# Kernel tuning notes

Hardware: AMD Instinct MI355X
Metric: run time of the kernel (lower is better)

The kernel has to match this reference:

```python
import jax, jax.numpy as jnp
import numpy as np

PERSON_DIM = 64
NUM_ZONES = 64
T_STEPS = 65536
N_EDGES = 512
H1, H2 = 128, 64
PENALTY = 1.0  # training_step=0 -> progress=0 -> penalty = min_penalty = 1.0


def build_adjacency(edge_index, num_zones):
    # symmetric 0/1 adjacency with self loops, as in set_graph_data
    A = jnp.zeros((num_zones, num_zones), jnp.float32)
    A = A.at[edge_index[0], edge_index[1]].set(1.0)
    A = A.at[edge_index[1], edge_index[0]].set(1.0)
    return jnp.maximum(A, jnp.eye(num_zones, dtype=jnp.float32))


def setup_inputs() -> dict:
    key = jax.random.key(0)
    ks = jax.random.split(key, 10)
    person_attrs = jax.random.normal(ks[0], (PERSON_DIM,), jnp.float32)
    times = jax.random.uniform(ks[1], (T_STEPS,), jnp.float32)
    zone_features = jax.random.normal(ks[2], (NUM_ZONES, 16), jnp.float32)
    edge_index = jax.random.randint(ks[3], (2, N_EDGES), 0, NUM_ZONES, jnp.int64 if jax.config.jax_enable_x64 else jnp.int32)
    din = PERSON_DIM + 1
    W1 = jax.random.normal(ks[4], (din, H1), jnp.float32) / np.sqrt(din)
    b1 = jnp.zeros((H1,), jnp.float32)
    W2 = jax.random.normal(ks[5], (H1, H2), jnp.float32) / np.sqrt(H1)
    b2 = jnp.zeros((H2,), jnp.float32)
    W3 = jax.random.normal(ks[6], (H2, NUM_ZONES), jnp.float32) / np.sqrt(H2)
    b3 = jnp.zeros((NUM_ZONES,), jnp.float32)
    return {"person_attrs": person_attrs, "times": times, "zone_features": zone_features,
            "edge_index": edge_index, "W1": W1, "b1": b1, "W2": W2, "b2": b2, "W3": W3, "b3": b3}


def reference(person_attrs, times, zone_features, edge_index, W1, b1, W2, b2, W3, b3):
    # MLP input per step = [person_attrs, time]; independent of the recurrence,
    # so batch the 3-layer MLP over all T timesteps (dropout in eval mode = identity).
    T = times.shape[0]
    x = jnp.concatenate([jnp.broadcast_to(person_attrs, (T, person_attrs.shape[0])),
                         times[:, None]], axis=-1)          # [T, D+1]
    h = jax.nn.relu(x @ W1 + b1)                              # [T, 128]
    h = jax.nn.relu(h @ W2 + b2)                              # [T, 64]
    raw_logits = h @ W3 + b3                                  # [T, Z]

    A = build_adjacency(edge_index, raw_logits.shape[-1])

    def step(current_zone, logits):
        constrained = logits - PENALTY * (1.0 - A[current_zone])
        return jnp.argmax(constrained), constrained

    _, zone_logits = jax.lax.scan(step, jnp.asarray(0, jnp.int32), raw_logits)
    return zone_logits  # [T, Z] (original also returns a None placeholder)
```

## Files before the change

kernel.cpp:

```cpp
#include <hip/hip_runtime.h>

#define T_STEPS 65536
#define NZ 64
#define NH1 128
#define NH2 64
#define NEDGE 512
#define NCHUNK 8192
#define CL 8
#define NSUPER 128
#define SUP_L 64

#define ADJ_OFF        0
#define BASE1_OFF      512
#define W1T_OFF        1536
#define NBRP_OFF       2560
#define DEGS_OFF       6656
#define CHUNKSTATE_OFF 6720
#define B2D_OFF        139264
#define B3D_OFF        139776
#define LG32_OFF       140288
#define FTAB_OFF       (LG32_OFF + (size_t)T_STEPS * NZ * 4)

#define CHUNKG_DOUT    0
#define SUPERS_DOUT    524288

typedef unsigned long long ull;
typedef unsigned int u32;
typedef unsigned char u8;
typedef double f64x4 __attribute__((ext_vector_type(4)));

__global__ void prep_kernel(const float* __restrict__ pa,
                            const int* __restrict__ edges,
                            const float* __restrict__ W1,
                            const float* __restrict__ b1,
                            const float* __restrict__ b2,
                            const float* __restrict__ b3,
                            unsigned char* ws) {
  ull* adj = (ull*)(ws + ADJ_OFF);
  double* base1 = (double*)(ws + BASE1_OFF);
  double* w1t   = (double*)(ws + W1T_OFF);
  double* b2d = (double*)(ws + B2D_OFF);
  double* b3d = (double*)(ws + B3D_OFF);
  int tid = threadIdx.x;
  if (tid < NZ) adj[tid] = 0ull;
  __syncthreads();
  if (tid < NEDGE) {
    int e0 = edges[tid];
    int e1 = edges[NEDGE + tid];
    atomicOr(&adj[e0], 1ull << e1);
    atomicOr(&adj[e1], 1ull << e0);
  }
  if (tid < NZ) atomicOr(&adj[tid], 1ull << tid);
  if (tid < NH1) {
    double acc = (double)b1[tid];
    for (int d = 0; d < 64; ++d)
      acc += (double)pa[d] * (double)W1[d * NH1 + tid];
    base1[tid] = acc;
    w1t[tid] = (double)W1[64 * NH1 + tid];
  }
  if (tid < NH2) b2d[tid] = (double)b2[tid];
  if (tid < NZ)  b3d[tid] = (double)b3[tid];
  __syncthreads();
  if (tid < NZ) {
    ull m = adj[tid];
    u32 wbuf[16];
    #pragma unroll
    for (int i = 0; i < 16; ++i) wbuf[i] = 0u;
    int deg = 0, jfirst = 0;
    while (m) {
      int j = __builtin_ctzll(m);
      m &= m - 1;
      if (deg == 0) jfirst = j;
      wbuf[deg >> 2] |= (u32)j << ((deg & 3) * 8);
      ++deg;
    }
    int padded = (deg + 3) & ~3;
    for (int k = deg; k < padded; ++k)
      wbuf[k >> 2] |= (u32)jfirst << ((k & 3) * 8);
    u32* np = (u32*)(ws + NBRP_OFF) + tid * 16;
    #pragma unroll
    for (int i = 0; i < 16; ++i) np[i] = wbuf[i];
    (ws + DEGS_OFF)[tid] = (u8)(padded >> 2);
  }
}

__global__ __launch_bounds__(512) void mlp_tables_kernel(
    const float* __restrict__ times,
    const float* __restrict__ W2,
    const float* __restrict__ W3,
    const unsigned char* __restrict__ ws_ro,
    float* __restrict__ lg32,
    unsigned char* __restrict__ chunkG,
    unsigned char* __restrict__ ftab) {
  __shared__ double region1[4224];
  __shared__ double region2[2112];
  __shared__ double base1s[NH1], w1ts[NH1];

  float* w2s = (float*)region1;
  float* w3s = (float*)region2;
  double* h2t = region1;
  double* lgT = region1;
  u8* F_lds = (u8*)region2;
  double* pv = (double*)((u8*)region2 + 4352);
  u8* pi = (u8*)region2 + 8448;

  const double* __restrict__ b2dg = (const double*)(ws_ro + B2D_OFF);
  const double* __restrict__ b3dg = (const double*)(ws_ro + B3D_OFF);

  int tid = threadIdx.x, lane = tid & 63, wv = tid >> 6;
  int i15 = lane & 15, g = lane >> 4;
  int mt = wv & 3, nt0 = (wv >> 2) * 2;
  int t0 = blockIdx.x * 64;

  for (int i = tid; i < NH1 * 64; i += 512) w2s[(i >> 6) * 66 + (i & 63)] = W2[i];
  for (int i = tid; i < NH2 * 64; i += 512) w3s[(i >> 6) * 66 + (i & 63)] = W3[i];
  if (tid < NH1) {
    base1s[tid] = ((const double*)(ws_ro + BASE1_OFF))[tid];
    w1ts[tid]   = ((const double*)(ws_ro + W1T_OFF))[tid];
  }
  double tv = (double)times[t0 + mt * 16 + i15];
  double bi20 = b2dg[nt0 * 16 + i15], bi21 = b2dg[nt0 * 16 + 16 + i15];
  double bi30 = b3dg[nt0 * 16 + i15], bi31 = b3dg[nt0 * 16 + 16 + i15];
  __syncthreads();

  f64x4 c0, c1;
  c0[0] = bi20; c0[1] = bi20; c0[2] = bi20; c0[3] = bi20;
  c1[0] = bi21; c1[1] = bi21; c1[2] = bi21; c1[3] = bi21;
  #pragma unroll 8
  for (int ks = 0; ks < 32; ++ks) {
    int h = ks * 4 + g;
    double a = fma(tv, w1ts[h], base1s[h]);
    a = a > 0.0 ? a : 0.0;
    double b0 = (double)w2s[h * 66 + nt0 * 16 + i15];
    double b1 = (double)w2s[h * 66 + nt0 * 16 + 16 + i15];
    c0 = __builtin_amdgcn_mfma_f64_16x16x4f64(a, b0, c0, 0, 0, 0);
    c1 = __builtin_amdgcn_mfma_f64_16x16x4f64(a, b1, c1, 0, 0, 0);
  }
  __syncthreads();
  #pragma unroll
  for (int r = 0; r < 4; ++r) {
    int t = mt * 16 + g * 4 + r;
    double v0 = c0[r] > 0.0 ? c0[r] : 0.0;
    double v1 = c1[r] > 0.0 ? c1[r] : 0.0;
    h2t[t * 66 + nt0 * 16 + i15] = v0;
    h2t[t * 66 + nt0 * 16 + 16 + i15] = v1;
  }
  __syncthreads();

  f64x4 d0, d1;
  d0[0] = bi30; d0[1] = bi30; d0[2] = bi30; d0[3] = bi30;
  d1[0] = bi31; d1[1] = bi31; d1[2] = bi31; d1[3] = bi31;
  #pragma unroll 8
  for (int ks = 0; ks < 16; ++ks) {
    int k = ks * 4 + g;
    double a3 = h2t[(mt * 16 + i15) * 66 + k];
    double b0 = (double)w3s[k * 66 + nt0 * 16 + i15];
    double b1 = (double)w3s[k * 66 + nt0 * 16 + 16 + i15];
    d0 = __builtin_amdgcn_mfma_f64_16x16x4f64(a3, b0, d0, 0, 0, 0);
    d1 = __builtin_amdgcn_mfma_f64_16x16x4f64(a3, b1, d1, 0, 0, 0);
  }
  __syncthreads();
  #pragma unroll
  for (int r = 0; r < 4; ++r) {
    int t = mt * 16 + g * 4 + r;
    int z0 = nt0 * 16 + i15, z1 = z0 + 16;
    lgT[z0 * 66 + t] = d0[r];
    lgT[z1 * 66 + t] = d1[r];
  }
  __syncthreads();

  {
    int zb = wv * 8;
    double vm = lgT[zb * 66 + lane];
    int jm = zb;
    lg32[(size_t)zb * T_STEPS + t0 + lane] = (float)vm;
    #pragma unroll
    for (int zz = 1; zz < 8; ++zz) {
      double v = lgT[(zb + zz) * 66 + lane];
      lg32[(size_t)(zb + zz) * T_STEPS + t0 + lane] = (float)v;
      if (v > vm) { vm = v; jm = zb + zz; }
    }
    pv[wv * 64 + lane] = vm;
    pi[wv * 64 + lane] = (u8)jm;
  }
  __syncthreads();
  double vmax = pv[lane];
  int jmax = pi[lane];
  #pragma unroll
  for (int w = 1; w < 8; ++w) {
    double v = pv[w * 64 + lane];
    int j = pi[w * 64 + lane];
    if (v > vmax) { vmax = v; jmax = j; }
  }
  double vgap = vmax - 1.0;

  const u32* __restrict__ nbrP = (const u32*)(ws_ro + NBRP_OFF);
  const u8* __restrict__ degs = ws_ro + DEGS_OFF;
  const ull* __restrict__ adjg = (const ull*)(ws_ro + ADJ_OFF);
  #pragma unroll
  for (int zz = 0; zz < 8; ++zz) {
    int z = __builtin_amdgcn_readfirstlane(wv * 8 + zz);
    ull az = adjg[z];
    int nk4 = __builtin_amdgcn_readfirstlane((int)degs[z]);
    double vn = -1.0e300;
    int jn = 0;
    for (int k4 = 0; k4 < nk4; ++k4) {
      u32 w4 = nbrP[z * 16 + k4];
      #pragma unroll
      for (int b = 0; b < 4; ++b) {
        int j = (w4 >> (b * 8)) & 63;
        double val = lgT[j * 66 + lane];
        if (val > vn) { vn = val; jn = j; }
      }
    }
    int bit = (int)((az >> jmax) & 1ull);
    int fnb = (vn > vgap) ? jn : ((vn < vgap) ? jmax : (jn < jmax ? jn : jmax));
    F_lds[lane * 68 + z] = (u8)(bit ? jmax : fnb);
  }
  __syncthreads();

  u32* fo = (u32*)(ftab + (size_t)t0 * 64);
  #pragma unroll
  for (int r = 0; r < 2; ++r) {
    int i = tid + r * 512;
    int t = i >> 4, z4 = (i & 15) << 2;
    fo[i] = *(const u32*)&F_lds[t * 68 + z4];
  }

  int c = blockIdx.x * 8 + wv;
  int cur = lane;
  #pragma unroll
  for (int i = 0; i < CL; ++i) cur = F_lds[(wv * 8 + i) * 68 + cur];
  chunkG[(size_t)c * 64 + lane] = (u8)cur;
}

__global__ __launch_bounds__(256) void super_compose_kernel(
    const unsigned char* __restrict__ chunkG,
    unsigned char* __restrict__ superS) {
  __shared__ u8 g[4][SUP_L * 64];
  int tid = threadIdx.x, lane = tid & 63, wv = tid >> 6;
  int k = blockIdx.x * 4 + wv;
  const u32* src = (const u32*)(chunkG + (size_t)k * SUP_L * 64);
  u32* dst = (u32*)g[wv];
  #pragma unroll 4
  for (int i = lane; i < SUP_L * 16; i += 64) dst[i] = src[i];
  int cur = lane;
  #pragma unroll 8
  for (int c = 0; c < SUP_L; ++c) {
    int gg = g[wv][c * 64 + lane];
    cur = __shfl(gg, cur, 64);
  }
  superS[(size_t)k * 64 + lane] = (u8)cur;
}

__global__ __launch_bounds__(256) void chunk_states_kernel(
    const unsigned char* __restrict__ chunkG,
    const unsigned char* __restrict__ superS,
    int* __restrict__ chunkState) {
  __shared__ unsigned char ssup[NSUPER * 64];
  __shared__ unsigned char g[4][SUP_L * 64];
  __shared__ int sbuf[4][SUP_L];
  int tid = threadIdx.x, lane = tid & 63, wv = tid >> 6;
  int k = blockIdx.x * 4 + wv;
  for (int i = tid; i < NSUPER * 16; i += 256)
    ((u32*)ssup)[i] = ((const u32*)superS)[i];
  const unsigned int* src = (const unsigned int*)(chunkG + (size_t)k * SUP_L * 64);
  unsigned int* dst = (unsigned int*)g[wv];
  #pragma unroll 4
  for (int i = lane; i < SUP_L * 16; i += 64) dst[i] = src[i];
  __syncthreads();
  int s = 0;
  for (int i = 0; i < k; ++i) s = ssup[i * 64 + s];
  for (int c = 0; c < SUP_L; ++c) {
    if (lane == 0) sbuf[wv][c] = s;
    s = g[wv][c * 64 + s];
  }
  chunkState[k * SUP_L + lane] = sbuf[wv][lane];
}

__global__ __launch_bounds__(256) void finalize_kernel(
    const float* __restrict__ lg32, const unsigned char* __restrict__ ws_ro,
    const int* __restrict__ chunkState, const unsigned char* __restrict__ ftab,
    float* __restrict__ out) {
  __shared__ ull adjs[64];
  __shared__ unsigned char fstage[4][CL * 64];
  int tid = threadIdx.x, lane = tid & 63, wv = tid >> 6;
  if (tid < 64) adjs[tid] = ((const ull*)(ws_ro + ADJ_OFF))[tid];
  __syncthreads();
  int c = blockIdx.x * 4 + wv;
  int s = chunkState[c];
  size_t tb = (size_t)c * CL * 64;

  float lgv[CL];
  #pragma unroll
  for (int i = 0; i < CL; ++i)
    lgv[i] = lg32[(size_t)lane * T_STEPS + c * CL + i];

  unsigned int* dst = (unsigned int*)fstage[wv];
  const unsigned int* src = (const unsigned int*)(ftab + tb);
  #pragma unroll
  for (int i = lane; i < CL * 16; i += 64) dst[i] = src[i];
  #pragma unroll
  for (int i = 0; i < CL; ++i) {
    int bit = (int)((adjs[s] >> lane) & 1ull);
    out[tb + i * 64 + lane] = bit ? lgv[i] : lgv[i] - 1.0f;
    s = fstage[wv][i * 64 + s];
  }
}

extern "C" void kernel_launch(void* const* d_in, const int* in_sizes, int n_in,
                              void* d_out, int out_size, void* d_ws, size_t ws_size,
                              hipStream_t stream) {
  const float* pa    = (const float*)d_in[0];
  const float* times = (const float*)d_in[1];
  const int*   edges = (const int*)d_in[3];
  const float* W1    = (const float*)d_in[4];
  const float* b1    = (const float*)d_in[5];
  const float* W2    = (const float*)d_in[6];
  const float* b2    = (const float*)d_in[7];
  const float* W3    = (const float*)d_in[8];
  const float* b3    = (const float*)d_in[9];

  unsigned char* ws = (unsigned char*)d_ws;
  unsigned char* outb = (unsigned char*)d_out;
  float* lg32 = (float*)(ws + LG32_OFF);
  unsigned char* ftab = ws + FTAB_OFF;
  unsigned char* chunkG = outb + CHUNKG_DOUT;
  unsigned char* superS = outb + SUPERS_DOUT;
  int* chunkState = (int*)(ws + CHUNKSTATE_OFF);

  hipLaunchKernelGGL(prep_kernel, dim3(1), dim3(512), 0, stream,
                     pa, edges, W1, b1, b2, b3, ws);
  hipLaunchKernelGGL(mlp_tables_kernel, dim3(T_STEPS / 64), dim3(512), 0, stream,
                     times, W2, W3, ws, lg32, chunkG, ftab);
  hipLaunchKernelGGL(super_compose_kernel, dim3(NSUPER / 4), dim3(256), 0, stream,
                     chunkG, superS);
  hipLaunchKernelGGL(chunk_states_kernel, dim3(NSUPER / 4), dim3(256), 0, stream,
                     chunkG, superS, chunkState);
  hipLaunchKernelGGL(finalize_kernel, dim3(NCHUNK / 4), dim3(256), 0, stream,
                     lg32, ws, chunkState, ftab, (float*)d_out);
}
```

Before: 91.13 us.

## Fuse chunk-state resolution into finalize kernel and move scratch tables to workspace

```diff
diff --git a/kernel.cpp b/kernel.cpp
--- a/kernel.cpp
+++ b/kernel.cpp
@@ -15,14 +15,12 @@
 #define W1T_OFF        1536
 #define NBRP_OFF       2560
 #define DEGS_OFF       6656
-#define CHUNKSTATE_OFF 6720
 #define B2D_OFF        139264
 #define B3D_OFF        139776
 #define LG32_OFF       140288
 #define FTAB_OFF       (LG32_OFF + (size_t)T_STEPS * NZ * 4)
-
-#define CHUNKG_DOUT    0
-#define SUPERS_DOUT    524288
+#define CHUNKG_WS      (FTAB_OFF + (size_t)T_STEPS * NZ)
+#define SUPERS_WS      (CHUNKG_WS + (size_t)NCHUNK * 64)
 
 typedef unsigned long long ull;
 typedef unsigned int u32;
@@ -84,7 +82,7 @@
   }
 }
 
-__global__ __launch_bounds__(512) void mlp_tables_kernel(
+__global__ __launch_bounds__(512, 6) void mlp_tables_kernel(
     const float* __restrict__ times,
     const float* __restrict__ W2,
     const float* __restrict__ W3,
@@ -253,58 +251,65 @@
   superS[(size_t)k * 64 + lane] = (u8)cur;
 }
 
-__global__ __launch_bounds__(256) void chunk_states_kernel(
+__global__ __launch_bounds__(256) void states_finalize_kernel(
+    const float* __restrict__ lg32, const unsigned char* __restrict__ ws_ro,
     const unsigned char* __restrict__ chunkG,
     const unsigned char* __restrict__ superS,
-    int* __restrict__ chunkState) {
-  __shared__ unsigned char ssup[NSUPER * 64];
-  __shared__ unsigned char g[4][SUP_L * 64];
-  __shared__ int sbuf[4][SUP_L];
+    const unsigned char* __restrict__ ftab,
+    float* __restrict__ out) {
+  __shared__ u8 region[NSUPER * 64];
+  __shared__ ull adjs[64];
+  __shared__ u8 fstage[4][2][CL * 64];
   int tid = threadIdx.x, lane = tid & 63, wv = tid >> 6;
-  int k = blockIdx.x * 4 + wv;
+  int b = blockIdx.x;
+  int k = b >> 3;
+  int myc = b * 8 + wv * 2;
+
+  if (tid < 64) adjs[tid] = ((const ull*)(ws_ro + ADJ_OFF))[tid];
   for (int i = tid; i < NSUPER * 16; i += 256)
-    ((u32*)ssup)[i] = ((const u32*)superS)[i];
-  const unsigned int* src = (const unsigned int*)(chunkG + (size_t)k * SUP_L * 64);
-  unsigned int* dst = (unsigned int*)g[wv];
-  #pragma unroll 4
-  for (int i = lane; i < SUP_L * 16; i += 64) dst[i] = src[i];
-  __syncthreads();
+    ((u32*)region)[i] = ((const u32*)superS)[i];
+  float lgv[2][CL];
+  #pragma unroll
+  for (int cc = 0; cc < 2; ++cc)
+    #pragma unroll
+    for (int i = 0; i < CL; ++i)
+      lgv[cc][i] = lg32[(size_t)lane * T_STEPS + (myc + cc) * CL + i];
+  #pragma unroll
+  for (int cc = 0; cc < 2; ++cc)
+    for (int i = lane; i < CL * 16; i += 64)
+      ((u32*)fstage[wv][cc])[i] =
+          ((const u32*)(ftab + (size_t)(myc + cc) * CL * 64))[i];
+  __syncthreads();
+
   int s = 0;
-  for (int i = 0; i < k; ++i) s = ssup[i * 64 + s];
-  for (int c = 0; c < SUP_L; ++c) {
-    if (lane == 0) sbuf[wv][c] = s;
-    s = g[wv][c * 64 + s];
-  }
-  chunkState[k * SUP_L + lane] = sbuf[wv][lane];
-}
-
-__global__ __launch_bounds__(256) void finalize_kernel(
-    const float* __restrict__ lg32, const unsigned char* __restrict__ ws_ro,
-    const int* __restrict__ chunkState, const unsigned char* __restrict__ ftab,
-    float* __restrict__ out) {
-  __shared__ ull adjs[64];
-  __shared__ unsigned char fstage[4][CL * 64];
-  int tid = threadIdx.x, lane = tid & 63, wv = tid >> 6;
-  if (tid < 64) adjs[tid] = ((const ull*)(ws_ro + ADJ_OFF))[tid];
-  __syncthreads();
-  int c = blockIdx.x * 4 + wv;
-  int s = chunkState[c];
-  size_t tb = (size_t)c * CL * 64;
-
-  float lgv[CL];
-  #pragma unroll
-  for (int i = 0; i < CL; ++i)
-    lgv[i] = lg32[(size_t)lane * T_STEPS + c * CL + i];
-
-  unsigned int* dst = (unsigned int*)fstage[wv];
-  const unsigned int* src = (const unsigned int*)(ftab + tb);
-  #pragma unroll
-  for (int i = lane; i < CL * 16; i += 64) dst[i] = src[i];
-  #pragma unroll
-  for (int i = 0; i < CL; ++i) {
-    int bit = (int)((adjs[s] >> lane) & 1ull);
-    out[tb + i * 64 + lane] = bit ? lgv[i] : lgv[i] - 1.0f;
-    s = fstage[wv][i * 64 + s];
+  for (int i = 0; i < k; ++i) s = region[i * 64 + s];
+  __syncthreads();
+  {
+    const u32* cg = (const u32*)(chunkG + (size_t)k * SUP_L * 64);
+    for (int i = tid; i < SUP_L * 16; i += 256) ((u32*)region)[i] = cg[i];
+  }
+  __syncthreads();
+  int lc0 = (b & 7) * 8;
+  for (int c = 0; c < lc0; ++c) s = region[c * 64 + s];
+  int e0 = 0, e1 = 0;
+  #pragma unroll
+  for (int j = 0; j < 8; ++j) {
+    if (j == wv * 2) e0 = s;
+    if (j == wv * 2 + 1) e1 = s;
+    s = region[(lc0 + j) * 64 + s];
+  }
+
+  #pragma unroll
+  for (int cc = 0; cc < 2; ++cc) {
+    int st = cc ? e1 : e0;
+    size_t tb = (size_t)(myc + cc) * CL * 64;
+    #pragma unroll
+    for (int i = 0; i < CL; ++i) {
+      int bit = (int)((adjs[st] >> lane) & 1ull);
+      float v = lgv[cc][i];
+      out[tb + i * 64 + lane] = bit ? v : v - 1.0f;
+      st = fstage[wv][cc][i * 64 + st];
+    }
   }
 }
 
@@ -322,12 +327,10 @@
   const float* b3    = (const float*)d_in[9];
 
   unsigned char* ws = (unsigned char*)d_ws;
-  unsigned char* outb = (unsigned char*)d_out;
   float* lg32 = (float*)(ws + LG32_OFF);
   unsigned char* ftab = ws + FTAB_OFF;
-  unsigned char* chunkG = outb + CHUNKG_DOUT;
-  unsigned char* superS = outb + SUPERS_DOUT;
-  int* chunkState = (int*)(ws + CHUNKSTATE_OFF);
+  unsigned char* chunkG = ws + CHUNKG_WS;
+  unsigned char* superS = ws + SUPERS_WS;
 
   hipLaunchKernelGGL(prep_kernel, dim3(1), dim3(512), 0, stream,
                      pa, edges, W1, b1, b2, b3, ws);
@@ -335,8 +338,6 @@
                      times, W2, W3, ws, lg32, chunkG, ftab);
   hipLaunchKernelGGL(super_compose_kernel, dim3(NSUPER / 4), dim3(256), 0, stream,
                      chunkG, superS);
-  hipLaunchKernelGGL(chunk_states_kernel, dim3(NSUPER / 4), dim3(256), 0, stream,
-                     chunkG, superS, chunkState);
-  hipLaunchKernelGGL(finalize_kernel, dim3(NCHUNK / 4), dim3(256), 0, stream,
-                     lg32, ws, chunkState, ftab, (float*)d_out);
-}
+  hipLaunchKernelGGL(states_finalize_kernel, dim3(NCHUNK / 8), dim3(256), 0, stream,
+                     lg32, ws, chunkG, superS, ftab, (float*)d_out);
+}
```

After: 83.91 us. 1.09x faster.
